# Performance work log

Hardware: AMD Instinct MI355X
Metric: run time of the kernel (lower is better)

## Reference

```python
import jax, jax.numpy as jnp
import numpy as np

BLANK_IDX = -1  # resolves to V-1
BATCH_FIRST = False
IS_PROBS = False


def setup_inputs() -> dict:
    key = jax.random.key(0)
    k1, k2 = jax.random.split(key)
    T, N, V = 2048, 32, 1024
    logits = jax.random.normal(k1, (T, N, V), dtype=jnp.float32)
    in_lens = jax.random.randint(k2, (N,), 1, T + 1).astype(jnp.int64)
    return {"logits": logits, "in_lens": in_lens}


def reference(logits, in_lens):
    # logits: (T, N, V) since batch_first=False
    V = logits.shape[2]
    blank = (BLANK_IDX + V) % V  # = V - 1
    logp = jax.nn.log_softmax(logits, axis=2)
    x = jnp.transpose(logp, (1, 0, 2))  # (N, T, V)
    max_ = jnp.max(x, axis=2)            # (N, T)
    argmax = jnp.argmax(x, axis=2)       # (N, T)
    N, T = argmax.shape

    keep = argmax != blank
    dedup = jnp.concatenate(
        [keep[:, :1], keep[:, 1:] & (argmax[:, 1:] != argmax[:, :-1])], axis=1
    )
    in_len_mask = jnp.arange(T)[None, :] < in_lens[:, None]  # (N, T)
    keep = dedup & in_len_mask
    max_ = jnp.where(in_len_mask, max_, 0.0)

    out_lens = keep.sum(axis=1)  # (N,)
    # stream compaction: position of each kept token within its row
    pos = jnp.cumsum(keep, axis=1) - 1               # (N, T)
    safe_pos = jnp.where(keep, pos, T)               # out-of-bounds -> dropped
    rows = jnp.broadcast_to(jnp.arange(N)[:, None], (N, T))
    # torch masked_scatter_ semantics: overwrite first out_lens[n] slots,
    # leave remaining entries as original argmax values ("undefined" region)
    paths = argmax.at[rows, safe_pos].set(argmax, mode="drop")

    max_total = max_.sum(axis=1)  # (N,)
    if not BATCH_FIRST:
        paths = paths.T  # (T, N)
    return max_total, paths, out_lens
```

## Files before the change

kernel.cpp:

```cpp
#include <hip/hip_runtime.h>


#define WAVE 64

typedef float fvec4 __attribute__((ext_vector_type(4)));
typedef int   ivec4 __attribute__((ext_vector_type(4)));

template <int CH>
__global__ __launch_bounds__(256) void row_lse_kernel(
    const float* __restrict__ logits,
    float* __restrict__ rmaxT, int* __restrict__ rargT,
    float* __restrict__ out_paths,
    int T, int N, int rows) {
  const int lane = threadIdx.x & (WAVE - 1);
  const int w    = threadIdx.x >> 6;
  const int V = CH * 256;
  const int wstride = gridDim.x * 4;

  for (int row = blockIdx.x * 4 + w; row < rows; row += wstride) {
    const fvec4* p4 = (const fvec4*)(logits + (size_t)row * V);

    float m = -3.4e38f;
    int   mi = 0;
    fvec4 v[CH];
#pragma unroll
    for (int c = 0; c < CH; ++c) {
      v[c] = p4[c * 64 + lane];
      const int idx = c * 256 + lane * 4;
      if (v[c].x > m) { m = v[c].x; mi = idx; }
      if (v[c].y > m) { m = v[c].y; mi = idx + 1; }
      if (v[c].z > m) { m = v[c].z; mi = idx + 2; }
      if (v[c].w > m) { m = v[c].w; mi = idx + 3; }
    }
#pragma unroll
    for (int off = 32; off; off >>= 1) {
      const float om = __shfl_down(m, off);
      const int   oi = __shfl_down(mi, off);
      if (om > m || (om == m && oi < mi)) { m = om; mi = oi; }
    }
    m = __shfl(m, 0);

    float s = 0.f;
#pragma unroll
    for (int c = 0; c < CH; ++c)
      s += __expf(v[c].x - m) + __expf(v[c].y - m) +
           __expf(v[c].z - m) + __expf(v[c].w - m);
#pragma unroll
    for (int off = 32; off; off >>= 1) s += __shfl_down(s, off);

    if (lane == 0) {
      const int t = row / N, n = row % N;
      rmaxT[(size_t)n * T + t] = -__logf(s);
      rargT[(size_t)n * T + t] = mi;
      out_paths[row] = (float)mi;
    }
  }
}

__global__ __launch_bounds__(256) void row_lse_generic(
    const float* __restrict__ logits,
    float* __restrict__ rmaxT, int* __restrict__ rargT,
    float* __restrict__ out_paths,
    int T, int N, int V, int rows) {
  const int lane = threadIdx.x & (WAVE - 1);
  const int w    = threadIdx.x >> 6;
  const int wstride = gridDim.x * 4;

  for (int row = blockIdx.x * 4 + w; row < rows; row += wstride) {
    const float* p = logits + (size_t)row * V;

    float m = -3.4e38f; int mi = 0;
    for (int i = lane; i < V; i += WAVE) {
      const float x = p[i];
      if (x > m) { m = x; mi = i; }
    }
    for (int off = 32; off; off >>= 1) {
      const float om = __shfl_down(m, off);
      const int   oi = __shfl_down(mi, off);
      if (om > m || (om == m && oi < mi)) { m = om; mi = oi; }
    }
    m = __shfl(m, 0);
    float s = 0.f;
    for (int i = lane; i < V; i += WAVE) s += __expf(p[i] - m);
    for (int off = 32; off; off >>= 1) s += __shfl_down(s, off);

    if (lane == 0) {
      const int t = row / N, n = row % N;
      rmaxT[(size_t)n * T + t] = -__logf(s);
      rargT[(size_t)n * T + t] = mi;
      out_paths[row] = (float)mi;
    }
  }
}

#define CB 256

template <int ITEMS>
__global__ __launch_bounds__(CB) void ctc_compact_fast(
    const float* __restrict__ rmaxT, const int* __restrict__ rargT,
    const int* __restrict__ in_lens, float* __restrict__ out,
    int T, int N, int V) {
  const int n = blockIdx.x;
  const int tid = threadIdx.x;
  const int L = in_lens[n];
  const int blank = V - 1;
  const int t0 = tid * ITEMS;

  float* out_total = out;
  float* out_paths = out + N;
  float* out_lens  = out + N + (size_t)T * N;

  const float* rm = rmaxT + (size_t)n * T;
  const int*   ra = rargT + (size_t)n * T;

  int   a[ITEMS];
  float mv[ITEMS];
#pragma unroll
  for (int i = 0; i < ITEMS; i += 4) {
    *(ivec4*)(a + i)  = *(const ivec4*)(ra + t0 + i);
    *(fvec4*)(mv + i) = *(const fvec4*)(rm + t0 + i);
  }

  __shared__ int   s_last[CB];
  __shared__ int   s_cnt[CB];
  __shared__ float s_sum[CB];
  s_last[tid] = a[ITEMS - 1];
  __syncthreads();
  int prev = (tid > 0) ? s_last[tid - 1] : -1;

  bool keep[ITEMS];
  int   cnt = 0;
  float sum = 0.f;
#pragma unroll
  for (int i = 0; i < ITEMS; ++i) {
    const int t = t0 + i;
    keep[i] = (t < L) && (a[i] != blank) && (a[i] != prev);
    prev = a[i];
    cnt += keep[i] ? 1 : 0;
    sum += (t < L) ? mv[i] : 0.f;
  }

  s_cnt[tid] = cnt;
  s_sum[tid] = sum;
  __syncthreads();
  for (int off = 1; off < CB; off <<= 1) {
    const int   c  = (tid >= off) ? s_cnt[tid - off] : 0;
    const float sv = (tid >= off) ? s_sum[tid - off] : 0.f;
    __syncthreads();
    s_cnt[tid] += c;
    s_sum[tid] += sv;
    __syncthreads();
  }
  if (tid == 0) {
    out_total[n] = s_sum[CB - 1];
    out_lens[n]  = (float)s_cnt[CB - 1];
  }

  int pos = s_cnt[tid] - cnt;
#pragma unroll
  for (int i = 0; i < ITEMS; ++i) {
    if (keep[i]) {
      out_paths[(size_t)pos * N + n] = (float)a[i];
      ++pos;
    }
  }
}

__global__ __launch_bounds__(CB) void ctc_compact_kernel(
    const float* __restrict__ rmaxT, const int* __restrict__ rargT,
    const int* __restrict__ in_lens, float* __restrict__ out,
    int T, int N, int V) {
  const int n = blockIdx.x;
  const int tid = threadIdx.x;
  const int L = in_lens[n];
  const int blank = V - 1;
  const int items = (T + CB - 1) / CB;
  const int t0 = tid * items;

  float* out_total = out;
  float* out_paths = out + N;
  float* out_lens  = out + N + (size_t)T * N;

  const float* rm = rmaxT + (size_t)n * T;
  const int*   ra = rargT + (size_t)n * T;

  int   cnt = 0;
  float sum = 0.f;
  int prev = (t0 > 0 && t0 <= T) ? ra[t0 - 1] : -1;
  for (int i = 0; i < items; ++i) {
    const int t = t0 + i;
    if (t >= T) break;
    const int a = ra[t];
    const bool keep = (t < L) && (a != blank) && (t == 0 || a != prev);
    prev = a;
    cnt += keep ? 1 : 0;
    if (t < L) sum += rm[t];
  }

  __shared__ int   s_cnt[CB];
  __shared__ float s_sum[CB];
  s_cnt[tid] = cnt;
  s_sum[tid] = sum;
  __syncthreads();
  for (int off = 1; off < CB; off <<= 1) {
    const int   c  = (tid >= off) ? s_cnt[tid - off] : 0;
    const float sv = (tid >= off) ? s_sum[tid - off] : 0.f;
    __syncthreads();
    s_cnt[tid] += c;
    s_sum[tid] += sv;
    __syncthreads();
  }
  const int prefix = s_cnt[tid] - cnt;
  if (tid == 0) {
    out_total[n] = s_sum[CB - 1];
    out_lens[n]  = (float)s_cnt[CB - 1];
  }

  int pos = prefix;
  prev = (t0 > 0 && t0 <= T) ? ra[t0 - 1] : -1;
  for (int i = 0; i < items; ++i) {
    const int t = t0 + i;
    if (t >= T) break;
    const int a = ra[t];
    const bool keep = (t < L) && (a != blank) && (t == 0 || a != prev);
    prev = a;
    if (keep) {
      out_paths[(size_t)pos * N + n] = (float)a;
      ++pos;
    }
  }
}

extern "C" void kernel_launch(void* const* d_in, const int* in_sizes, int n_in,
                              void* d_out, int out_size, void* d_ws, size_t ws_size,
                              hipStream_t stream) {
  const float* logits = (const float*)d_in[0];
  const int* in_lens  = (const int*)d_in[1];
  float* out = (float*)d_out;

  const int N = in_sizes[1];
  const int T = (out_size - 2 * N) / N;
  const long long total = in_sizes[0];
  const int V = (int)(total / ((long long)T * N));
  const int rows = T * N;

  float* rmaxT = (float*)d_ws;
  int*   rargT = (int*)((char*)d_ws + (size_t)rows * sizeof(float));
  float* out_paths = out + N;

  int grid1 = (rows + 3) / 4;
  if (grid1 > 2048) grid1 = 2048;

  if (V == 1024) {
    row_lse_kernel<4><<<grid1, 256, 0, stream>>>(logits, rmaxT, rargT, out_paths, T, N, rows);
  } else if (V == 512) {
    row_lse_kernel<2><<<grid1, 256, 0, stream>>>(logits, rmaxT, rargT, out_paths, T, N, rows);
  } else if (V == 2048) {
    row_lse_kernel<8><<<grid1, 256, 0, stream>>>(logits, rmaxT, rargT, out_paths, T, N, rows);
  } else {
    row_lse_generic<<<grid1, 256, 0, stream>>>(logits, rmaxT, rargT, out_paths, T, N, V, rows);
  }

  if (T == CB * 8) {
    ctc_compact_fast<8><<<N, CB, 0, stream>>>(rmaxT, rargT, in_lens, out, T, N, V);
  } else {
    ctc_compact_kernel<<<N, CB, 0, stream>>>(rmaxT, rargT, in_lens, out, T, N, V);
  }
}
```

Baseline: 359.2 us.

## Process two rows per wave with nontemporal loads and one-shot grid

The row log-softmax kernel drops the grid-stride loop and launches one block per eight rows, with each wave handling two rows so that eight vector loads are in flight per lane. Logit loads use nontemporal hints. The per-row max and argmax are packed into one 8-byte struct and written once, and the compaction kernel reads them back as pairs. Path outputs are staged in shared memory so each block writes them with a few threads instead of scattered lane-0 stores. The aim is more memory-level parallelism on a bandwidth-bound read of 256 MB, at the cost of more registers per lane and a much larger grid.

```diff
diff --git a/kernel.cpp b/kernel.cpp
--- a/kernel.cpp
+++ b/kernel.cpp
@@ -6,90 +6,129 @@
 typedef float fvec4 __attribute__((ext_vector_type(4)));
 typedef int   ivec4 __attribute__((ext_vector_type(4)));
 
+struct alignas(8) MA { float m; int a; };
+
 template <int CH>
-__global__ __launch_bounds__(256) void row_lse_kernel(
+__global__ __launch_bounds__(256, 8) void row_lse_kernel(
     const float* __restrict__ logits,
-    float* __restrict__ rmaxT, int* __restrict__ rargT,
+    MA* __restrict__ rpairT,
     float* __restrict__ out_paths,
     int T, int N, int rows) {
   const int lane = threadIdx.x & (WAVE - 1);
   const int w    = threadIdx.x >> 6;
   const int V = CH * 256;
-  const int wstride = gridDim.x * 4;
-
-  for (int row = blockIdx.x * 4 + w; row < rows; row += wstride) {
-    const fvec4* p4 = (const fvec4*)(logits + (size_t)row * V);
-
-    float m = -3.4e38f;
-    int   mi = 0;
-    fvec4 v[CH];
-#pragma unroll
-    for (int c = 0; c < CH; ++c) {
-      v[c] = p4[c * 64 + lane];
-      const int idx = c * 256 + lane * 4;
-      if (v[c].x > m) { m = v[c].x; mi = idx; }
-      if (v[c].y > m) { m = v[c].y; mi = idx + 1; }
-      if (v[c].z > m) { m = v[c].z; mi = idx + 2; }
-      if (v[c].w > m) { m = v[c].w; mi = idx + 3; }
+  const int rowA = blockIdx.x * 8 + w * 2;
+  const int rowB = rowA + 1;
+  const bool aA = rowA < rows, aB = rowB < rows;
+  const fvec4* pA = (const fvec4*)(logits + (size_t)(aA ? rowA : 0) * V);
+  const fvec4* pB = (const fvec4*)(logits + (size_t)(aB ? rowB : 0) * V);
+
+  fvec4 vA[CH], vB[CH];
+#pragma unroll
+  for (int c = 0; c < CH; ++c) {
+    vA[c] = __builtin_nontemporal_load(pA + c * 64 + lane);
+    vB[c] = __builtin_nontemporal_load(pB + c * 64 + lane);
+  }
+
+  float mA = -3.4e38f, mB = -3.4e38f;
+  int   iA = 0,        iB = 0;
+#pragma unroll
+  for (int c = 0; c < CH; ++c) {
+    const int idx = c * 256 + lane * 4;
+    if (vA[c].x > mA) { mA = vA[c].x; iA = idx; }
+    if (vA[c].y > mA) { mA = vA[c].y; iA = idx + 1; }
+    if (vA[c].z > mA) { mA = vA[c].z; iA = idx + 2; }
+    if (vA[c].w > mA) { mA = vA[c].w; iA = idx + 3; }
+    if (vB[c].x > mB) { mB = vB[c].x; iB = idx; }
+    if (vB[c].y > mB) { mB = vB[c].y; iB = idx + 1; }
+    if (vB[c].z > mB) { mB = vB[c].z; iB = idx + 2; }
+    if (vB[c].w > mB) { mB = vB[c].w; iB = idx + 3; }
+  }
+#pragma unroll
+  for (int off = 32; off; off >>= 1) {
+    const float omA = __shfl_down(mA, off);
+    const int   oiA = __shfl_down(iA, off);
+    const float omB = __shfl_down(mB, off);
+    const int   oiB = __shfl_down(iB, off);
+    if (omA > mA || (omA == mA && oiA < iA)) { mA = omA; iA = oiA; }
+    if (omB > mB || (omB == mB && oiB < iB)) { mB = omB; iB = oiB; }
+  }
+  mA = __shfl(mA, 0);
+  mB = __shfl(mB, 0);
+
+  float sA = 0.f, sB = 0.f;
+#pragma unroll
+  for (int c = 0; c < CH; ++c) {
+    sA += __expf(vA[c].x - mA) + __expf(vA[c].y - mA) +
+          __expf(vA[c].z - mA) + __expf(vA[c].w - mA);
+    sB += __expf(vB[c].x - mB) + __expf(vB[c].y - mB) +
+          __expf(vB[c].z - mB) + __expf(vB[c].w - mB);
+  }
+#pragma unroll
+  for (int off = 32; off; off >>= 1) {
+    sA += __shfl_down(sA, off);
+    sB += __shfl_down(sB, off);
+  }
+
+  __shared__ float s_path[8];
+  if (lane == 0) {
+    if (aA) {
+      const int t = rowA / N, n = rowA % N;
+      MA r; r.m = -__logf(sA); r.a = iA;
+      rpairT[(size_t)n * T + t] = r;
+      s_path[w * 2] = (float)iA;
     }
-#pragma unroll
-    for (int off = 32; off; off >>= 1) {
-      const float om = __shfl_down(m, off);
-      const int   oi = __shfl_down(mi, off);
-      if (om > m || (om == m && oi < mi)) { m = om; mi = oi; }
+    if (aB) {
+      const int t = rowB / N, n = rowB % N;
+      MA r; r.m = -__logf(sB); r.a = iB;
+      rpairT[(size_t)n * T + t] = r;
+      s_path[w * 2 + 1] = (float)iB;
     }
-    m = __shfl(m, 0);
-
-    float s = 0.f;
-#pragma unroll
-    for (int c = 0; c < CH; ++c)
-      s += __expf(v[c].x - m) + __expf(v[c].y - m) +
-           __expf(v[c].z - m) + __expf(v[c].w - m);
-#pragma unroll
-    for (int off = 32; off; off >>= 1) s += __shfl_down(s, off);
-
-    if (lane == 0) {
-      const int t = row / N, n = row % N;
-      rmaxT[(size_t)n * T + t] = -__logf(s);
-      rargT[(size_t)n * T + t] = mi;
-      out_paths[row] = (float)mi;
-    }
+  }
+  __syncthreads();
+  if (threadIdx.x < 8) {
+    const int r = blockIdx.x * 8 + threadIdx.x;
+    if (r < rows) out_paths[r] = s_path[threadIdx.x];
   }
 }
 
 __global__ __launch_bounds__(256) void row_lse_generic(
     const float* __restrict__ logits,
-    float* __restrict__ rmaxT, int* __restrict__ rargT,
+    MA* __restrict__ rpairT,
     float* __restrict__ out_paths,
     int T, int N, int V, int rows) {
   const int lane = threadIdx.x & (WAVE - 1);
   const int w    = threadIdx.x >> 6;
-  const int wstride = gridDim.x * 4;
-
-  for (int row = blockIdx.x * 4 + w; row < rows; row += wstride) {
-    const float* p = logits + (size_t)row * V;
-
-    float m = -3.4e38f; int mi = 0;
-    for (int i = lane; i < V; i += WAVE) {
-      const float x = p[i];
-      if (x > m) { m = x; mi = i; }
-    }
-    for (int off = 32; off; off >>= 1) {
-      const float om = __shfl_down(m, off);
-      const int   oi = __shfl_down(mi, off);
-      if (om > m || (om == m && oi < mi)) { m = om; mi = oi; }
-    }
-    m = __shfl(m, 0);
-    float s = 0.f;
-    for (int i = lane; i < V; i += WAVE) s += __expf(p[i] - m);
-    for (int off = 32; off; off >>= 1) s += __shfl_down(s, off);
-
-    if (lane == 0) {
-      const int t = row / N, n = row % N;
-      rmaxT[(size_t)n * T + t] = -__logf(s);
-      rargT[(size_t)n * T + t] = mi;
-      out_paths[row] = (float)mi;
-    }
+  const int row  = blockIdx.x * 4 + w;
+  const bool active = row < rows;
+  const float* p = logits + (size_t)(active ? row : 0) * V;
+
+  float m = -3.4e38f; int mi = 0;
+  for (int i = lane; i < V; i += WAVE) {
+    const float x = p[i];
+    if (x > m) { m = x; mi = i; }
+  }
+  for (int off = 32; off; off >>= 1) {
+    const float om = __shfl_down(m, off);
+    const int   oi = __shfl_down(mi, off);
+    if (om > m || (om == m && oi < mi)) { m = om; mi = oi; }
+  }
+  m = __shfl(m, 0);
+  float s = 0.f;
+  for (int i = lane; i < V; i += WAVE) s += __expf(p[i] - m);
+  for (int off = 32; off; off >>= 1) s += __shfl_down(s, off);
+
+  __shared__ float s_path[4];
+  if (lane == 0 && active) {
+    const int t = row / N, n = row % N;
+    MA r; r.m = -__logf(s); r.a = mi;
+    rpairT[(size_t)n * T + t] = r;
+    s_path[w] = (float)mi;
+  }
+  __syncthreads();
+  if (threadIdx.x < 4) {
+    const int r = blockIdx.x * 4 + threadIdx.x;
+    if (r < rows) out_paths[r] = s_path[threadIdx.x];
   }
 }
 
@@ -97,7 +136,7 @@
 
 template <int ITEMS>
 __global__ __launch_bounds__(CB) void ctc_compact_fast(
-    const float* __restrict__ rmaxT, const int* __restrict__ rargT,
+    const MA* __restrict__ rpairT,
     const int* __restrict__ in_lens, float* __restrict__ out,
     int T, int N, int V) {
   const int n = blockIdx.x;
@@ -110,15 +149,15 @@
   float* out_paths = out + N;
   float* out_lens  = out + N + (size_t)T * N;
 
-  const float* rm = rmaxT + (size_t)n * T;
-  const int*   ra = rargT + (size_t)n * T;
+  const MA* rp = rpairT + (size_t)n * T;
 
   int   a[ITEMS];
   float mv[ITEMS];
 #pragma unroll
-  for (int i = 0; i < ITEMS; i += 4) {
-    *(ivec4*)(a + i)  = *(const ivec4*)(ra + t0 + i);
-    *(fvec4*)(mv + i) = *(const fvec4*)(rm + t0 + i);
+  for (int i = 0; i < ITEMS; i += 2) {
+    const ivec4 q = *(const ivec4*)(rp + t0 + i);
+    mv[i]     = __int_as_float(q.x); a[i]     = q.y;
+    mv[i + 1] = __int_as_float(q.z); a[i + 1] = q.w;
   }
 
   __shared__ int   s_last[CB];
@@ -167,7 +206,7 @@
 }
 
 __global__ __launch_bounds__(CB) void ctc_compact_kernel(
-    const float* __restrict__ rmaxT, const int* __restrict__ rargT,
+    const MA* __restrict__ rpairT,
     const int* __restrict__ in_lens, float* __restrict__ out,
     int T, int N, int V) {
   const int n = blockIdx.x;
@@ -181,20 +220,19 @@
   float* out_paths = out + N;
   float* out_lens  = out + N + (size_t)T * N;
 
-  const float* rm = rmaxT + (size_t)n * T;
-  const int*   ra = rargT + (size_t)n * T;
+  const MA* rp = rpairT + (size_t)n * T;
 
   int   cnt = 0;
   float sum = 0.f;
-  int prev = (t0 > 0 && t0 <= T) ? ra[t0 - 1] : -1;
+  int prev = (t0 > 0 && t0 <= T) ? rp[t0 - 1].a : -1;
   for (int i = 0; i < items; ++i) {
     const int t = t0 + i;
     if (t >= T) break;
-    const int a = ra[t];
+    const int a = rp[t].a;
     const bool keep = (t < L) && (a != blank) && (t == 0 || a != prev);
     prev = a;
     cnt += keep ? 1 : 0;
-    if (t < L) sum += rm[t];
+    if (t < L) sum += rp[t].m;
   }
 
   __shared__ int   s_cnt[CB];
@@ -217,11 +255,11 @@
   }
 
   int pos = prefix;
-  prev = (t0 > 0 && t0 <= T) ? ra[t0 - 1] : -1;
+  prev = (t0 > 0 && t0 <= T) ? rp[t0 - 1].a : -1;
   for (int i = 0; i < items; ++i) {
     const int t = t0 + i;
     if (t >= T) break;
-    const int a = ra[t];
+    const int a = rp[t].a;
     const bool keep = (t < L) && (a != blank) && (t == 0 || a != prev);
     prev = a;
     if (keep) {
@@ -244,26 +282,25 @@
   const int V = (int)(total / ((long long)T * N));
   const int rows = T * N;
 
-  float* rmaxT = (float*)d_ws;
-  int*   rargT = (int*)((char*)d_ws + (size_t)rows * sizeof(float));
+  MA* rpairT = (MA*)d_ws;
   float* out_paths = out + N;
 
-  int grid1 = (rows + 3) / 4;
-  if (grid1 > 2048) grid1 = 2048;
+  const int grid1 = (rows + 7) / 8;
 
   if (V == 1024) {
-    row_lse_kernel<4><<<grid1, 256, 0, stream>>>(logits, rmaxT, rargT, out_paths, T, N, rows);
+    row_lse_kernel<4><<<grid1, 256, 0, stream>>>(logits, rpairT, out_paths, T, N, rows);
   } else if (V == 512) {
-    row_lse_kernel<2><<<grid1, 256, 0, stream>>>(logits, rmaxT, rargT, out_paths, T, N, rows);
+    row_lse_kernel<2><<<grid1, 256, 0, stream>>>(logits, rpairT, out_paths, T, N, rows);
   } else if (V == 2048) {
-    row_lse_kernel<8><<<grid1, 256, 0, stream>>>(logits, rmaxT, rargT, out_paths, T, N, rows);
+    row_lse_kernel<8><<<grid1, 256, 0, stream>>>(logits, rpairT, out_paths, T, N, rows);
   } else {
-    row_lse_generic<<<grid1, 256, 0, stream>>>(logits, rmaxT, rargT, out_paths, T, N, V, rows);
+    const int gridg = (rows + 3) / 4;
+    row_lse_generic<<<gridg, 256, 0, stream>>>(logits, rpairT, out_paths, T, N, V, rows);
   }
 
   if (T == CB * 8) {
-    ctc_compact_fast<8><<<N, CB, 0, stream>>>(rmaxT, rargT, in_lens, out, T, N, V);
+    ctc_compact_fast<8><<<N, CB, 0, stream>>>(rpairT, in_lens, out, T, N, V);
   } else {
-    ctc_compact_kernel<<<N, CB, 0, stream>>>(rmaxT, rargT, in_lens, out, T, N, V);
-  }
-}
+    ctc_compact_kernel<<<N, CB, 0, stream>>>(rpairT, in_lens, out, T, N, V);
+  }
+}
```

Measured after the change: 332.8 us. 1.08x faster.
